# Performance work log

Hardware: AMD Instinct MI355X
Metric: run time of the kernel (lower is better)

Reference implementation:

```python
import jax, jax.numpy as jnp
import numpy as np

B, D, G, P = 4, 768, 64, 256
H = 12
HD = D // H
SCALE = HD ** -0.5


def setup_inputs() -> dict:
    key = jax.random.key(0)
    k1, k2, k3, k4 = jax.random.split(key, 4)
    x = jax.random.normal(k1, (B, D, G, P), dtype=jnp.float32)
    # per-group patch-patch mask; p=0.9 keep so no row is fully masked in practice
    mask = jax.random.bernoulli(k2, 0.9, (G, P, P))
    w_qkv = jax.random.normal(k3, (3 * D, D), dtype=jnp.float32) * (D ** -0.5)
    w_proj = jax.random.normal(k4, (D, D), dtype=jnp.float32) * (D ** -0.5)
    b_proj = jnp.zeros((D,), dtype=jnp.float32)
    return {"x": x, "mask": mask, "w_qkv": w_qkv, "w_proj": w_proj, "b_proj": b_proj}


def reference(x, mask, w_qkv, w_proj, b_proj):
    # 1x1 conv == channel matmul: [B,D,G,P] -> [B,3D,G,P]
    qkv = jnp.einsum('bdgp,ed->begp', x, w_qkv)
    # channel layout is (qkv, head, head_dim)
    qkv = qkv.reshape(B, 3, H, HD, G, P)
    qkv = jnp.transpose(qkv, (1, 0, 2, 4, 5, 3))  # [3, B, H, G, P, HD]
    q, k, v = qkv[0], qkv[1], qkv[2]
    attn = jnp.einsum('bhgpd,bhgqd->bhgpq', q, k) * SCALE  # [B,H,G,P,P]
    mask_value = -jnp.finfo(attn.dtype).max
    attn = jnp.where(mask[None, None], attn, mask_value)
    attn = jax.nn.softmax(attn, axis=-1)
    out = jnp.einsum('bhgpq,bhgqd->bhgpd', attn, v)  # [B,H,G,P,HD]
    out = jnp.transpose(out, (0, 1, 4, 2, 3)).reshape(B, D, G, P)
    out = jnp.einsum('bdgp,ed->begp', out, w_proj) + b_proj[None, :, None, None]
    return out
```

## Files before the change

### kernel.cpp

```cpp
#include <hip/hip_runtime.h>
#include <float.h>

#define D_    768
#define GD    64
#define PD    256
#define HH    12
#define HDD   64
#define NGP   (GD*PD)
#define NB    4
#define SCALE 0.125f
#define QPRE  (0.125f * 1.44269504f)

typedef __bf16 bf16x8 __attribute__((ext_vector_type(8)));
typedef __bf16 bf16x4 __attribute__((ext_vector_type(4)));
typedef _Float16 f16x8 __attribute__((ext_vector_type(8)));
typedef _Float16 f16x4 __attribute__((ext_vector_type(4)));
typedef float  f32x4  __attribute__((ext_vector_type(4)));

__device__ __forceinline__ float exp2_fast(float x) {
  return __builtin_amdgcn_exp2f(x);
}

__device__ __forceinline__ void gload_lds16(const __bf16* g, __bf16* l) {
  __builtin_amdgcn_global_load_lds(
      (const __attribute__((address_space(1))) void*)g,
      (__attribute__((address_space(3))) void*)l, 16, 0, 0);
}

__device__ __forceinline__ unsigned short f2bf_bits(float f) {
  __bf16 h = (__bf16)f;
  unsigned short u;
  __builtin_memcpy(&u, &h, 2);
  return u;
}

__global__ void wcast_k(const float* __restrict__ in, __bf16* __restrict__ out, int n,
                        int nscale, float sc) {
  int i = (blockIdx.x * 256 + threadIdx.x) * 4;
  if (i >= n) return;
  float s = (i < nscale) ? sc : 1.f;
  float4 v = *(const float4*)(in + i);
  bf16x4 o;
  o[0] = (__bf16)(v.x * s); o[1] = (__bf16)(v.y * s);
  o[2] = (__bf16)(v.z * s); o[3] = (__bf16)(v.w * s);
  *(bf16x4*)(out + i) = o;
}

__global__ void maskpack_k(const unsigned char* __restrict__ mask, unsigned* __restrict__ gbm) {
  const int g = blockIdx.x, p = threadIdx.x;
  const unsigned* mwords = (const unsigned*)mask;
  bool is_i32 = true;
  #pragma unroll
  for (int i = 0; i < 16; ++i) is_i32 = is_i32 && (mwords[i] <= 1u);
  unsigned* o = gbm + ((size_t)g * PD + p) * 8;
  if (is_i32) {
    const uint4* mr4 = (const uint4*)(mwords + ((size_t)g * PD + p) * PD);
    #pragma unroll
    for (int w = 0; w < 8; ++w) {
      unsigned bits = 0;
      #pragma unroll
      for (int j = 0; j < 8; ++j) {
        uint4 m4 = mr4[w*8 + j];
        bits |= (m4.x ? 1u : 0u) << (j*4+0);
        bits |= (m4.y ? 1u : 0u) << (j*4+1);
        bits |= (m4.z ? 1u : 0u) << (j*4+2);
        bits |= (m4.w ? 1u : 0u) << (j*4+3);
      }
      o[w] = bits;
    }
  } else {
    const unsigned* mr = (const unsigned*)(mask + ((size_t)g * PD + p) * PD);
    #pragma unroll
    for (int w = 0; w < 8; ++w) {
      unsigned bits = 0;
      #pragma unroll
      for (int j = 0; j < 8; ++j) {
        unsigned vv = mr[w*8 + j];
        if (vv & 0x000000FFu) bits |= 1u << (j*4+0);
        if (vv & 0x0000FF00u) bits |= 1u << (j*4+1);
        if (vv & 0x00FF0000u) bits |= 1u << (j*4+2);
        if (vv & 0xFF000000u) bits |= 1u << (j*4+3);
      }
      o[w] = bits;
    }
  }
}

__global__ void tcast_k(const float* __restrict__ in, __bf16* __restrict__ out) {
  __shared__ float s[32][66];
  const int tid = threadIdx.x;
  const int c0 = blockIdx.x * 64;
  const int r0 = blockIdx.y * 32;
  const float* inz = in + (size_t)blockIdx.z * D_ * NGP;
  unsigned* outu = (unsigned*)out + (size_t)blockIdx.z * NGP * (D_ / 2);
  const int lx = tid & 63, ly = tid >> 6;
  #pragma unroll
  for (int rr = 0; rr < 32; rr += 4)
    s[rr + ly][lx] = inz[(size_t)(r0 + rr + ly) * NGP + c0 + lx];
  __syncthreads();
  const int wx = tid & 15, wy = tid >> 4;
  #pragma unroll
  for (int p = 0; p < 64; p += 16) {
    int j = p + wy;
    unsigned pk = (unsigned)f2bf_bits(s[2*wx][j]) |
                  ((unsigned)f2bf_bits(s[2*wx+1][j]) << 16);
    outu[(size_t)(c0 + j) * (D_/2) + (r0 >> 1) + wx] = pk;
  }
}

template<int BIAS, int OUT, int OUTB>
__global__ __launch_bounds__(256, 2)
void mfma_gemm(const __bf16* __restrict__ A, const __bf16* __restrict__ Bt,
               const float* __restrict__ bias, void* __restrict__ Cout,
               int M, int N, int K) {
  __shared__ __align__(16) __bf16 As[128 * 64];
  __shared__ __align__(16) __bf16 Bs[128 * 64];
  const int tid = threadIdx.x;
  const int wave = tid >> 6, lane = tid & 63;
  const int wm = wave >> 1, wn = wave & 1;
  const int m0 = blockIdx.y * 128, n0 = blockIdx.x * 128;

  const int r0g = wave * 2, r1g = wave * 2 + 1;
  const int kch = (lane >> 4) * 8;
  const __bf16* gA0 = A  + (size_t)(m0 + r0g * 16 + (lane & 15)) * K + kch;
  const __bf16* gA1 = gA0 + (size_t)16 * K;
  const __bf16* gB0 = Bt + (size_t)(n0 + r0g * 16 + (lane & 15)) * K + kch;
  const __bf16* gB1 = gB0 + (size_t)16 * K;
  __bf16* lA0 = As + r0g * 1024;  __bf16* lA1 = As + r1g * 1024;
  __bf16* lB0 = Bs + r0g * 1024;  __bf16* lB1 = Bs + r1g * 1024;

  f32x4 acc[4][4] = {};
  const bf16x8* Av = (const bf16x8*)As;
  const bf16x8* Bv = (const bf16x8*)Bs;

  for (int k0 = 0; k0 < K; k0 += 64) {
    __syncthreads();
    gload_lds16(gA0, lA0);  gload_lds16(gA0 + 32, lA0 + 512);
    gload_lds16(gA1, lA1);  gload_lds16(gA1 + 32, lA1 + 512);
    gload_lds16(gB0, lB0);  gload_lds16(gB0 + 32, lB0 + 512);
    gload_lds16(gB1, lB1);  gload_lds16(gB1 + 32, lB1 + 512);
    gA0 += 64; gA1 += 64; gB0 += 64; gB1 += 64;
    __syncthreads();
    #pragma unroll
    for (int s = 0; s < 2; ++s) {
      bf16x8 af[4], bf[4];
      #pragma unroll
      for (int i = 0; i < 4; ++i) af[i] = Av[(wm * 4 + i) * 128 + s * 64 + lane];
      #pragma unroll
      for (int j = 0; j < 4; ++j) bf[j] = Bv[(wn * 4 + j) * 128 + s * 64 + lane];
      #pragma unroll
      for (int i = 0; i < 4; ++i)
        #pragma unroll
        for (int j = 0; j < 4; ++j)
          acc[i][j] = __builtin_amdgcn_mfma_f32_16x16x32_bf16(af[i], bf[j], acc[i][j], 0, 0, 0);
    }
  }

  #pragma unroll
  for (int i = 0; i < 4; ++i) {
    #pragma unroll
    for (int j = 0; j < 4; ++j) {
      const int col  = n0 + wn * 64 + j * 16 + (lane & 15);
      const int row0 = m0 + wm * 64 + i * 16 + (lane >> 4) * 4;
      #pragma unroll
      for (int r = 0; r < 4; ++r) {
        float v = acc[i][j][r];
        if (BIAS) v += bias[row0 + r];
        if (OUT == 1)
          ((__bf16*)Cout)[(size_t)(row0 + r) * N + col] = (__bf16)v;
        else if (OUT == 2)
          ((_Float16*)Cout)[(size_t)(row0 + r) * N + col] = (_Float16)v;
        else if (OUTB) {
          const int bb = col >> 14, gp = col & (NGP - 1);
          ((float*)Cout)[((size_t)bb * D_ + row0 + r) * NGP + gp] = v;
        } else
          ((float*)Cout)[(size_t)(row0 + r) * N + col] = v;
      }
    }
  }
}

__global__ __launch_bounds__(256, 2)
void attn_mfma(const __bf16* __restrict__ qkT, const _Float16* __restrict__ vbuf,
               const unsigned* __restrict__ gbm, __bf16* __restrict__ aot,
               int vcols) {
  __shared__ unsigned mb[256][9];
  __shared__ __align__(16) _Float16 p_lds[4][4096];

  const int g = blockIdx.x, h = blockIdx.y, b = blockIdx.z;
  const int tid = threadIdx.x;
  const int wave = tid >> 6, lane = tid & 63;
  const int l15 = lane & 15, t4 = lane >> 4;

  const __bf16* qk = qkT + (size_t)b * NGP * 1536;

  const __bf16* qbase = qk + (size_t)(g*PD + wave*64 + l15) * 1536 + h*HDD + t4*8;
  bf16x8 qf[4][2];
  #pragma unroll
  for (int j = 0; j < 4; ++j)
    #pragma unroll
    for (int ks = 0; ks < 2; ++ks)
      qf[j][ks] = *(const bf16x8*)(qbase + (size_t)j*16*1536 + ks*32);

  {
    const uint4* gbr = (const uint4*)(gbm + ((size_t)g * PD + tid) * 8);
    uint4 w0 = gbr[0], w1 = gbr[1];
    mb[tid][0] = w0.x; mb[tid][1] = w0.y; mb[tid][2] = w0.z; mb[tid][3] = w0.w;
    mb[tid][4] = w1.x; mb[tid][5] = w1.y; mb[tid][6] = w1.z; mb[tid][7] = w1.w;
  }
  __syncthreads();

  const __bf16* kbase = qk + (size_t)(g*PD + l15) * 1536 + D_ + h*HDD + t4*8;
  const _Float16* vb  = vbuf + (size_t)(h*HDD + l15) * vcols + (size_t)b*NGP + g*PD + t4*8;
  _Float16* pw = &p_lds[wave][0];

  float rm[4], rl[4];
  #pragma unroll
  for (int j = 0; j < 4; ++j) { rm[j] = -1e30f; rl[j] = 0.f; }
  f32x4 o[4][4] = {};

  for (int qt = 0; qt < 4; ++qt) {
    bf16x8 kf[4][2];
    #pragma unroll
    for (int i = 0; i < 4; ++i)
      #pragma unroll
      for (int ks = 0; ks < 2; ++ks)
        kf[i][ks] = *(const bf16x8*)(kbase + (size_t)(qt*64 + i*16)*1536 + ks*32);
    f32x4 s[4][4] = {};
    #pragma unroll
    for (int ks = 0; ks < 2; ++ks)
      #pragma unroll
      for (int i = 0; i < 4; ++i)
        #pragma unroll
        for (int j = 0; j < 4; ++j)
          s[i][j] = __builtin_amdgcn_mfma_f32_16x16x32_bf16(kf[i][ks], qf[j][ks], s[i][j], 0, 0, 0);

    f16x8 vf[4][2];
    #pragma unroll
    for (int i2 = 0; i2 < 4; ++i2)
      #pragma unroll
      for (int ks = 0; ks < 2; ++ks)
        vf[i2][ks] = *(const f16x8*)(vb + (size_t)i2*16*vcols + qt*64 + ks*32);

    #pragma unroll
    for (int j = 0; j < 4; ++j) {
      const int pl = wave*64 + j*16 + l15;
      const unsigned w0 = mb[pl][qt*2 + 0], w1 = mb[pl][qt*2 + 1];
      float mxj = -1e30f;
      #pragma unroll
      for (int i = 0; i < 4; ++i) {
        const unsigned w = (i < 2) ? w0 : w1;
        const int base = (i & 1)*16 + t4*4;
        #pragma unroll
        for (int r = 0; r < 4; ++r) {
          float sv = ((w >> (base + r)) & 1u) ? s[i][j][r] : -1e30f;
          s[i][j][r] = sv;
          mxj = fmaxf(mxj, sv);
        }
      }
      mxj = fmaxf(mxj, __shfl_xor(mxj, 16, 64));
      mxj = fmaxf(mxj, __shfl_xor(mxj, 32, 64));
      const bool defer = __all(mxj <= rm[j] + 8.f);
      const float mnew = defer ? rm[j] : fmaxf(rm[j], mxj);
      const float mneg = -mnew;
      float rs = 0.f;
      #pragma unroll
      for (int i = 0; i < 4; ++i)
        #pragma unroll
        for (int r = 0; r < 4; ++r) {
          float e = exp2_fast(s[i][j][r] + mneg);
          s[i][j][r] = e;
          rs += e;
        }
      rs += __shfl_xor(rs, 16, 64);
      rs += __shfl_xor(rs, 32, 64);
      if (defer) {
        rl[j] += rs;
      } else {
        const float scl = exp2_fast(rm[j] - mnew);
        rl[j] = fmaf(rl[j], scl, rs);
        #pragma unroll
        for (int i2 = 0; i2 < 4; ++i2)
          #pragma unroll
          for (int r = 0; r < 4; ++r)
            o[i2][j][r] *= scl;
        rm[j] = mnew;
      }
      #pragma unroll
      for (int i = 0; i < 4; ++i) {
        f16x4 pk;
        #pragma unroll
        for (int r = 0; r < 4; ++r) pk[r] = (_Float16)s[i][j][r];
        *(f16x4*)&pw[j*1024 + (2*i + (t4 >> 1))*128 + l15*8 + 4*(t4 & 1)] = pk;
      }
    }

    f16x8 pf[4][2];
    #pragma unroll
    for (int j2 = 0; j2 < 4; ++j2)
      #pragma unroll
      for (int ks = 0; ks < 2; ++ks)
        pf[j2][ks] = *(const f16x8*)&pw[j2*1024 + (4*ks + t4)*128 + l15*8];
    #pragma unroll
    for (int ks = 0; ks < 2; ++ks)
      #pragma unroll
      for (int i2 = 0; i2 < 4; ++i2)
        #pragma unroll
        for (int j2 = 0; j2 < 4; ++j2)
          o[i2][j2] = __builtin_amdgcn_mfma_f32_16x16x32_f16(vf[i2][ks], pf[j2][ks], o[i2][j2], 0, 0, 0);
  }

  #pragma unroll
  for (int j2 = 0; j2 < 4; ++j2) {
    const float inv = 1.f / rl[j2];
    __bf16* ao = aot + ((size_t)b*NGP + g*PD + wave*64 + j2*16 + l15) * D_ + h*HDD;
    #pragma unroll
    for (int i2 = 0; i2 < 4; ++i2) {
      bf16x4 ov;
      #pragma unroll
      for (int r = 0; r < 4; ++r) ov[r] = (__bf16)(o[i2][j2][r] * inv);
      *(bf16x4*)(ao + i2*16 + t4*4) = ov;
    }
  }
}

extern "C" void kernel_launch(void* const* d_in, const int* in_sizes, int n_in,
                              void* d_out, int out_size, void* d_ws, size_t ws_size,
                              hipStream_t stream) {
  const float* x      = (const float*)d_in[0];
  const unsigned char* mask = (const unsigned char*)d_in[1];
  const float* w_qkv  = (const float*)d_in[2];
  const float* w_proj = (const float*)d_in[3];
  const float* b_proj = (const float*)d_in[4];
  float* out = (float*)d_out;

  const size_t sz_qkT = (size_t)NB * NGP * 1536 * 2;
  const size_t sz_v   = (size_t)D_ * NB * NGP * 2;
  const size_t sz_xt  = (size_t)NB * NGP * D_ * 2;
  const size_t sz_aot = (size_t)NB * NGP * D_ * 2;
  const size_t sz_wq  = (size_t)3 * D_ * D_ * 2;
  const size_t sz_wp  = (size_t)D_ * D_ * 2;
  const size_t sz_gbm = (size_t)GD * PD * 8 * 4;
  const size_t need_big = sz_qkT + sz_v + sz_xt + sz_aot + sz_wq + sz_wp + sz_gbm;

  const bool big = ws_size >= need_big;

  char* ws = (char*)d_ws;
  __bf16*   qkT  = (__bf16*)ws;    ws += big ? sz_qkT : (size_t)NGP*1536*2;
  _Float16* vf16 = (_Float16*)ws;  ws += big ? sz_v   : (size_t)D_*NGP*2;
  __bf16*   xt   = (__bf16*)ws;    ws += big ? sz_xt  : (size_t)NGP*D_*2;
  __bf16*   aot  = (__bf16*)ws;    ws += big ? sz_aot : (size_t)NGP*D_*2;
  __bf16*   wq_bf= (__bf16*)ws;    ws += sz_wq;
  __bf16*   wp_bf= (__bf16*)ws;    ws += sz_wp;
  unsigned* gbm  = (unsigned*)ws;

  wcast_k<<<(3*D_*D_)/1024, 256, 0, stream>>>(w_qkv,  wq_bf, 3*D_*D_, D_*D_, QPRE);
  wcast_k<<<(D_*D_)/1024,   256, 0, stream>>>(w_proj, wp_bf, D_*D_, 0, 1.f);
  maskpack_k<<<GD, PD, 0, stream>>>(mask, gbm);

  if (big) {
    const int NCOL = NB * NGP;
    tcast_k<<<dim3(NGP/64, D_/32, NB), 256, 0, stream>>>(x, xt);
    mfma_gemm<0,1,0><<<dim3(1536/128, NCOL/128), 256, 0, stream>>>(xt, wq_bf, nullptr, qkT, NCOL, 1536, D_);
    mfma_gemm<0,2,0><<<dim3(NCOL/128, D_/128), 256, 0, stream>>>(wq_bf + (size_t)1536*D_, xt, nullptr, vf16, D_, NCOL, D_);
    attn_mfma<<<dim3(GD, HH, NB), 256, 0, stream>>>(qkT, vf16, gbm, aot, NCOL);
    mfma_gemm<1,0,1><<<dim3(NCOL/128, D_/128), 256, 0, stream>>>(wp_bf, aot, b_proj, out, D_, NCOL, D_);
  } else {
    for (int b = 0; b < NB; ++b) {
      const float* xb = x + (size_t)b * D_ * NGP;
      float* ob = out + (size_t)b * D_ * NGP;
      tcast_k<<<dim3(NGP/64, D_/32, 1), 256, 0, stream>>>(xb, xt);
      mfma_gemm<0,1,0><<<dim3(1536/128, NGP/128), 256, 0, stream>>>(xt, wq_bf, nullptr, qkT, NGP, 1536, D_);
      mfma_gemm<0,2,0><<<dim3(NGP/128, D_/128), 256, 0, stream>>>(wq_bf + (size_t)1536*D_, xt, nullptr, vf16, D_, NGP, D_);
      attn_mfma<<<dim3(GD, HH, 1), 256, 0, stream>>>(qkT, vf16, gbm, aot, NGP);
      mfma_gemm<1,0,0><<<dim3(NGP/128, D_/128), 256, 0, stream>>>(wp_bf, aot, b_proj, ob, D_, NGP, D_);
    }
  }
}
```

Measured before the change: 1.075 ms.

## Double-buffer GEMM LDS tiles and remap workgroups for XCD/L2 locality

The GEMM kernel now stages K in 32-wide chunks into two LDS buffers, issuing the global-to-LDS loads for the next chunk while MFMAs run on the current one. This replaces the two-barrier load-then-compute loop. Workgroup IDs are remapped so consecutive IDs land on the same XCD, with M-fastest or N-fastest tile ordering selected per GEMM to improve cache reuse. Launch bounds rise to 4 blocks per CU, which may increase register pressure or spilling. Each iteration still waits on vmcnt(0) and a barrier, so the overlap is limited to one chunk.

```diff
diff --git a/kernel.cpp b/kernel.cpp
--- a/kernel.cpp
+++ b/kernel.cpp
@@ -108,17 +108,25 @@
   }
 }
 
-template<int BIAS, int OUT, int OUTB>
-__global__ __launch_bounds__(256, 2)
+template<int BIAS, int OUT, int OUTB, int MF>
+__global__ __launch_bounds__(256, 4)
 void mfma_gemm(const __bf16* __restrict__ A, const __bf16* __restrict__ Bt,
                const float* __restrict__ bias, void* __restrict__ Cout,
                int M, int N, int K) {
-  __shared__ __align__(16) __bf16 As[128 * 64];
-  __shared__ __align__(16) __bf16 Bs[128 * 64];
+  __shared__ __align__(16) __bf16 As[2][128 * 32];
+  __shared__ __align__(16) __bf16 Bs[2][128 * 32];
   const int tid = threadIdx.x;
   const int wave = tid >> 6, lane = tid & 63;
   const int wm = wave >> 1, wn = wave & 1;
-  const int m0 = blockIdx.y * 128, n0 = blockIdx.x * 128;
+
+  const int Gx = gridDim.x, Gy = gridDim.y;
+  int id = blockIdx.y * Gx + blockIdx.x;
+  const int nwg = Gx * Gy;
+  if ((nwg & 7) == 0) { const int c = nwg >> 3; id = (id & 7) * c + (id >> 3); }
+  int mt, nt;
+  if (MF) { mt = id % Gy; nt = id / Gy; }
+  else    { nt = id % Gx; mt = id / Gx; }
+  const int m0 = mt * 128, n0 = nt * 128;
 
   const int r0g = wave * 2, r1g = wave * 2 + 1;
   const int kch = (lane >> 4) * 8;
@@ -126,35 +134,42 @@
   const __bf16* gA1 = gA0 + (size_t)16 * K;
   const __bf16* gB0 = Bt + (size_t)(n0 + r0g * 16 + (lane & 15)) * K + kch;
   const __bf16* gB1 = gB0 + (size_t)16 * K;
-  __bf16* lA0 = As + r0g * 1024;  __bf16* lA1 = As + r1g * 1024;
-  __bf16* lB0 = Bs + r0g * 1024;  __bf16* lB1 = Bs + r1g * 1024;
 
   f32x4 acc[4][4] = {};
-  const bf16x8* Av = (const bf16x8*)As;
-  const bf16x8* Bv = (const bf16x8*)Bs;
-
-  for (int k0 = 0; k0 < K; k0 += 64) {
-    __syncthreads();
-    gload_lds16(gA0, lA0);  gload_lds16(gA0 + 32, lA0 + 512);
-    gload_lds16(gA1, lA1);  gload_lds16(gA1 + 32, lA1 + 512);
-    gload_lds16(gB0, lB0);  gload_lds16(gB0 + 32, lB0 + 512);
-    gload_lds16(gB1, lB1);  gload_lds16(gB1 + 32, lB1 + 512);
-    gA0 += 64; gA1 += 64; gB0 += 64; gB1 += 64;
-    __syncthreads();
-    #pragma unroll
-    for (int s = 0; s < 2; ++s) {
-      bf16x8 af[4], bf[4];
-      #pragma unroll
-      for (int i = 0; i < 4; ++i) af[i] = Av[(wm * 4 + i) * 128 + s * 64 + lane];
-      #pragma unroll
-      for (int j = 0; j < 4; ++j) bf[j] = Bv[(wn * 4 + j) * 128 + s * 64 + lane];
-      #pragma unroll
-      for (int i = 0; i < 4; ++i)
-        #pragma unroll
-        for (int j = 0; j < 4; ++j)
-          acc[i][j] = __builtin_amdgcn_mfma_f32_16x16x32_bf16(af[i], bf[j], acc[i][j], 0, 0, 0);
-    }
-  }
+
+#define STAGE_G(c, kb) do { \
+    gload_lds16(gA0 + (kb), &As[c][r0g * 512]); \
+    gload_lds16(gA1 + (kb), &As[c][r1g * 512]); \
+    gload_lds16(gB0 + (kb), &Bs[c][r0g * 512]); \
+    gload_lds16(gB1 + (kb), &Bs[c][r1g * 512]); \
+  } while (0)
+
+  STAGE_G(0, 0);
+  asm volatile("s_waitcnt vmcnt(0)" ::: "memory");
+  __builtin_amdgcn_s_barrier();
+  __builtin_amdgcn_sched_barrier(0);
+
+  int cur = 0;
+  for (int k0 = 0; k0 < K; k0 += 32) {
+    if (k0 + 32 < K) STAGE_G(cur ^ 1, k0 + 32);
+    const bf16x8* Av = (const bf16x8*)As[cur];
+    const bf16x8* Bv = (const bf16x8*)Bs[cur];
+    bf16x8 af[4], bf[4];
+    #pragma unroll
+    for (int i = 0; i < 4; ++i) af[i] = Av[(wm * 4 + i) * 64 + lane];
+    #pragma unroll
+    for (int j = 0; j < 4; ++j) bf[j] = Bv[(wn * 4 + j) * 64 + lane];
+    #pragma unroll
+    for (int i = 0; i < 4; ++i)
+      #pragma unroll
+      for (int j = 0; j < 4; ++j)
+        acc[i][j] = __builtin_amdgcn_mfma_f32_16x16x32_bf16(af[i], bf[j], acc[i][j], 0, 0, 0);
+    asm volatile("s_waitcnt vmcnt(0)" ::: "memory");
+    __builtin_amdgcn_s_barrier();
+    __builtin_amdgcn_sched_barrier(0);
+    cur ^= 1;
+  }
+#undef STAGE_G
 
   #pragma unroll
   for (int i = 0; i < 4; ++i) {
@@ -361,19 +376,19 @@
   if (big) {
     const int NCOL = NB * NGP;
     tcast_k<<<dim3(NGP/64, D_/32, NB), 256, 0, stream>>>(x, xt);
-    mfma_gemm<0,1,0><<<dim3(1536/128, NCOL/128), 256, 0, stream>>>(xt, wq_bf, nullptr, qkT, NCOL, 1536, D_);
-    mfma_gemm<0,2,0><<<dim3(NCOL/128, D_/128), 256, 0, stream>>>(wq_bf + (size_t)1536*D_, xt, nullptr, vf16, D_, NCOL, D_);
+    mfma_gemm<0,1,0,0><<<dim3(1536/128, NCOL/128), 256, 0, stream>>>(xt, wq_bf, nullptr, qkT, NCOL, 1536, D_);
+    mfma_gemm<0,2,0,1><<<dim3(NCOL/128, D_/128), 256, 0, stream>>>(wq_bf + (size_t)1536*D_, xt, nullptr, vf16, D_, NCOL, D_);
     attn_mfma<<<dim3(GD, HH, NB), 256, 0, stream>>>(qkT, vf16, gbm, aot, NCOL);
-    mfma_gemm<1,0,1><<<dim3(NCOL/128, D_/128), 256, 0, stream>>>(wp_bf, aot, b_proj, out, D_, NCOL, D_);
+    mfma_gemm<1,0,1,1><<<dim3(NCOL/128, D_/128), 256, 0, stream>>>(wp_bf, aot, b_proj, out, D_, NCOL, D_);
   } else {
     for (int b = 0; b < NB; ++b) {
       const float* xb = x + (size_t)b * D_ * NGP;
       float* ob = out + (size_t)b * D_ * NGP;
       tcast_k<<<dim3(NGP/64, D_/32, 1), 256, 0, stream>>>(xb, xt);
-      mfma_gemm<0,1,0><<<dim3(1536/128, NGP/128), 256, 0, stream>>>(xt, wq_bf, nullptr, qkT, NGP, 1536, D_);
-      mfma_gemm<0,2,0><<<dim3(NGP/128, D_/128), 256, 0, stream>>>(wq_bf + (size_t)1536*D_, xt, nullptr, vf16, D_, NGP, D_);
+      mfma_gemm<0,1,0,0><<<dim3(1536/128, NGP/128), 256, 0, stream>>>(xt, wq_bf, nullptr, qkT, NGP, 1536, D_);
+      mfma_gemm<0,2,0,1><<<dim3(NGP/128, D_/128), 256, 0, stream>>>(wq_bf + (size_t)1536*D_, xt, nullptr, vf16, D_, NGP, D_);
       attn_mfma<<<dim3(GD, HH, 1), 256, 0, stream>>>(qkT, vf16, gbm, aot, NGP);
-      mfma_gemm<1,0,0><<<dim3(NGP/128, D_/128), 256, 0, stream>>>(wp_bf, aot, b_proj, ob, D_, NGP, D_);
-    }
-  }
-}
+      mfma_gemm<1,0,0,1><<<dim3(NGP/128, D_/128), 256, 0, stream>>>(wp_bf, aot, b_proj, ob, D_, NGP, D_);
+    }
+  }
+}
```

Result: slower. 1.099 ms (+2.3%).
